# Performance work log

Measured on AMD Instinct MI355X. Metric: run time of the kernel, lower is better.

Reference implementation:

```python
import jax, jax.numpy as jnp
import numpy as np

VOL_SHAPE = (256, 256, 256)
DELTA = 1
EPS = 1e-8


def _radius_bins(shape, delta):
    # Frequency-index radius map (equivalent to distance from DC with fft wraparound),
    # binned into shells of width `delta`. Computed once with numpy (constant).
    axes = [np.fft.fftfreq(n) * n for n in shape]
    grids = np.meshgrid(*axes, indexing='ij')
    r = np.sqrt(sum(g.astype(np.float64) ** 2 for g in grids))
    bins = np.floor(r / delta).astype(np.int32)
    return bins.ravel(), int(bins.max()) + 1

_BINS, _NUM_SHELLS = _radius_bins(VOL_SHAPE, DELTA)
_BINS_J = jnp.asarray(_BINS)


def setup_inputs() -> dict:
    key = jax.random.key(0)
    kx, ky = jax.random.split(key)
    shp = (2, 1) + VOL_SHAPE
    X = jax.random.normal(kx, shp, dtype=jnp.float32)
    Y = jax.random.normal(ky, shp, dtype=jnp.float32)
    return {"X": X, "Y": Y}


def _fsc(X, Y):
    B, C = X.shape[0], X.shape[1]
    Fx = jnp.fft.fftn(X, axes=(-3, -2, -1))  # complex64 [B,C,D,H,W]
    Fy = jnp.fft.fftn(Y, axes=(-3, -2, -1))
    N = VOL_SHAPE[0] * VOL_SHAPE[1] * VOL_SHAPE[2]
    # Per-voxel quantities, flattened over the volume: [B*C, N]
    num = (Fx.real * Fy.real + Fx.imag * Fy.imag).reshape(B * C, N)  # Re(Fx * conj(Fy))
    px = (Fx.real ** 2 + Fx.imag ** 2).reshape(B * C, N)
    py = (Fy.real ** 2 + Fy.imag ** 2).reshape(B * C, N)
    seg = lambda v: jax.ops.segment_sum(v, _BINS_J, num_segments=_NUM_SHELLS)
    num_s = jax.vmap(seg)(num)  # [B*C, S]
    px_s = jax.vmap(seg)(px)
    py_s = jax.vmap(seg)(py)
    fsc = num_s / jnp.sqrt(px_s * py_s + EPS)  # [B*C, S]
    return fsc.reshape(B, C, _NUM_SHELLS)


def reference(X, Y):
    fsc = _fsc(X, Y)
    # size_average=True: average over radii, channel and batch -> scalar
    return jnp.mean(fsc)
```

## Files before the change

### kernel.cpp

```cpp
#include <hip/hip_runtime.h>
#include <math.h>

#define VOL (256 * 256 * 256)
#define NSHELL 222
#define SBINS 224
#define NSPLIT 16
#define PI_D 3.14159265358979323846
#define VSTRIDE ((size_t)129 << 16)

__device__ __forceinline__ int rev4(int e) {
  return ((e & 3) << 6) | (((e >> 2) & 3) << 4) | (((e >> 4) & 3) << 2) | ((e >> 6) & 3);
}

__global__ void tw_init(float2* __restrict__ gtw) {
  int t = threadIdx.x;
  double a = -2.0 * PI_D * (double)t / 256.0;
  gtw[t] = make_float2((float)cos(a), (float)sin(a));
}

__device__ __forceinline__ void bfly4_dif(float* re, float* im, const float* twr,
                                          const float* twi, int a0, int a1, int a2,
                                          int a3, int t1, int t2, int t3) {
  float x0r = re[a0], x0i = im[a0], x1r = re[a1], x1i = im[a1];
  float x2r = re[a2], x2i = im[a2], x3r = re[a3], x3i = im[a3];
  float s02r = x0r + x2r, s02i = x0i + x2i, d02r = x0r - x2r, d02i = x0i - x2i;
  float s13r = x1r + x3r, s13i = x1i + x3i, d13r = x1r - x3r, d13i = x1i - x3i;
  re[a0] = s02r + s13r; im[a0] = s02i + s13i;
  float c1r = d02r + d13i, c1i = d02i - d13r;
  re[a1] = c1r * twr[t1] - c1i * twi[t1]; im[a1] = c1r * twi[t1] + c1i * twr[t1];
  float c2r = s02r - s13r, c2i = s02i - s13i;
  re[a2] = c2r * twr[t2] - c2i * twi[t2]; im[a2] = c2r * twi[t2] + c2i * twr[t2];
  float c3r = d02r - d13i, c3i = d02i + d13r;
  re[a3] = c3r * twr[t3] - c3i * twi[t3]; im[a3] = c3r * twi[t3] + c3i * twr[t3];
}

__device__ __forceinline__ void seg_flush(float* sh, int sb, float nv, float pv,
                                          float qv, int l) {
#pragma unroll
  for (int d = 1; d < 64; d <<= 1) {
    int sbo = __shfl_down(sb, d);
    float no = __shfl_down(nv, d);
    float po = __shfl_down(pv, d);
    float qo = __shfl_down(qv, d);
    if (l + d < 64 && sbo == sb) { nv += no; pv += po; qv += qo; }
  }
  int sbp = __shfl_up(sb, 1);
  if (l == 0 || sbp != sb) {
    atomicAdd(&sh[3 * sb + 0], nv);
    atomicAdd(&sh[3 * sb + 1], pv);
    atomicAdd(&sh[3 * sb + 2], qv);
  }
}

__device__ __forceinline__ float2 cmul(float2 a, float2 b) {
  return make_float2(a.x * b.x - a.y * b.y, a.x * b.y + a.y * b.x);
}

__device__ __forceinline__ void fft16(float2* v) {
  const float C1 = 0.92387953251128674f;
  const float S1 = 0.38268343236508978f;
  const float R2 = 0.70710678118654752f;
  float2 s[16];
#pragma unroll
  for (int p = 0; p < 4; ++p) {
    float2 a = v[p], b = v[p + 4], cc = v[p + 8], d = v[p + 12];
    float2 t0 = make_float2(a.x + cc.x, a.y + cc.y);
    float2 t2 = make_float2(a.x - cc.x, a.y - cc.y);
    float2 t1 = make_float2(b.x + d.x, b.y + d.y);
    float2 t3 = make_float2(b.x - d.x, b.y - d.y);
    s[p]      = make_float2(t0.x + t1.x, t0.y + t1.y);
    s[p + 4]  = make_float2(t2.x + t3.y, t2.y - t3.x);
    s[p + 8]  = make_float2(t0.x - t1.x, t0.y - t1.y);
    s[p + 12] = make_float2(t2.x - t3.y, t2.y + t3.x);
  }
  s[5]  = cmul(s[5],  make_float2(C1, -S1));
  s[6]  = cmul(s[6],  make_float2(R2, -R2));
  s[7]  = cmul(s[7],  make_float2(S1, -C1));
  s[9]  = cmul(s[9],  make_float2(R2, -R2));
  s[10] = cmul(s[10], make_float2(0.f, -1.f));
  s[11] = cmul(s[11], make_float2(-R2, -R2));
  s[13] = cmul(s[13], make_float2(S1, -C1));
  s[14] = cmul(s[14], make_float2(-R2, -R2));
  s[15] = cmul(s[15], make_float2(-C1, S1));
#pragma unroll
  for (int r = 0; r < 4; ++r) {
    float2 u0 = s[4 * r], u1 = s[4 * r + 1], u2 = s[4 * r + 2], u3 = s[4 * r + 3];
    float2 e0 = make_float2(u0.x + u2.x, u0.y + u2.y);
    float2 e1 = make_float2(u0.x - u2.x, u0.y - u2.y);
    float2 o0 = make_float2(u1.x + u3.x, u1.y + u3.y);
    float2 o1 = make_float2(u1.x - u3.x, u1.y - u3.y);
    v[r]      = make_float2(e0.x + o0.x, e0.y + o0.y);
    v[4 + r]  = make_float2(e1.x + o1.y, e1.y - o1.x);
    v[8 + r]  = make_float2(e0.x - o0.x, e0.y - o0.y);
    v[12 + r] = make_float2(e1.x - o1.y, e1.y + o1.x);
  }
}

__global__ __launch_bounds__(256) void fft_z_pack(const float* __restrict__ X,
                                                  const float* __restrict__ Y,
                                                  float2* __restrict__ Gx,
                                                  float2* __restrict__ Gy,
                                                  const float2* __restrict__ gtw) {
  __shared__ float zr[256 * 17], zi[256 * 17];
  __shared__ float twr[256], twi[256];
  int t = threadIdx.x;
  { float2 w = gtw[t]; twr[t] = w.x; twi[t] = w.y; }
  int li = t >> 4, c = t & 15;
  int y = blockIdx.x >> 4;
  int x0 = (blockIdx.x & 15) << 4;
  const float4* xp = (const float4*)(X + (((size_t)(x0 + li)) << 16) + ((size_t)y << 8));
  const float4* yp = (const float4*)(Y + (((size_t)(x0 + li)) << 16) + ((size_t)y << 8));
#pragma unroll
  for (int it = 0; it < 4; ++it) {
    int e4 = c + 16 * it;
    float4 a = xp[e4];
    float4 b = yp[e4];
    int e = e4 << 2;
    zr[(e + 0) * 17 + li] = a.x; zi[(e + 0) * 17 + li] = b.x;
    zr[(e + 1) * 17 + li] = a.y; zi[(e + 1) * 17 + li] = b.y;
    zr[(e + 2) * 17 + li] = a.z; zi[(e + 2) * 17 + li] = b.z;
    zr[(e + 3) * 17 + li] = a.w; zi[(e + 3) * 17 + li] = b.w;
  }
  __syncthreads();
#pragma unroll
  for (int s = 0; s < 4; ++s) {
    int M = 64 >> (2 * s);
    int F = 1 << (2 * s);
#pragma unroll
    for (int ib = 0; ib < 4; ++ib) {
      int j = c + 16 * ib;
      int p = j & (M - 1);
      int jb = j >> (6 - 2 * s);
      int base = jb * (M << 2) + p;
      bfly4_dif(zr, zi, twr, twi, base * 17 + li, (base + M) * 17 + li,
                (base + 2 * M) * 17 + li, (base + 3 * M) * 17 + li,
                (p * F) & 255, (2 * p * F) & 255, (3 * p * F) & 255);
    }
    __syncthreads();
  }
  int krow = t >> 4, xi = t & 15;
#pragma unroll
  for (int g = 0; g < 9; ++g) {
    int kz = g * 16 + krow;
    if (kz <= 128) {
      int s1 = rev4(kz & 255);
      int s2 = rev4((256 - kz) & 255);
      float ar = zr[s1 * 17 + xi], ai = zi[s1 * 17 + xi];
      float br = zr[s2 * 17 + xi], bi = zi[s2 * 17 + xi];
      size_t off = ((size_t)kz << 16) + ((size_t)y << 8) + (size_t)(x0 + xi);
      Gx[off] = make_float2(0.5f * (ar + br), 0.5f * (ai - bi));
      Gy[off] = make_float2(0.5f * (ai + bi), 0.5f * (br - ar));
    }
  }
}

__global__ __launch_bounds__(256, 4) void fft_y(float2* __restrict__ G,
                                                const float2* __restrict__ gtw) {
  __shared__ float2 scr[16 * 273];
  int t = threadIdx.x;
  int xi = t & 15, h = t >> 4;
  int x0 = blockIdx.x << 4;
  int kz = blockIdx.y;
  float2* Gp = G + (size_t)blockIdx.z * VSTRIDE + ((size_t)kz << 16) + (size_t)(x0 + xi);
  float2 v[16];
#pragma unroll
  for (int m = 0; m < 16; ++m) v[m] = Gp[(size_t)((m << 4) | h) << 8];
  fft16(v);
#pragma unroll
  for (int k1 = 1; k1 < 16; ++k1) v[k1] = cmul(v[k1], gtw[h * k1]);
  int wb = xi * 273 + h * 17;
#pragma unroll
  for (int k1 = 0; k1 < 16; ++k1) scr[wb + k1] = v[k1];
  __syncthreads();
  float2 u[16];
  int rb = xi * 273 + h;
#pragma unroll
  for (int j2 = 0; j2 < 16; ++j2) u[j2] = scr[rb + j2 * 17];
  fft16(u);
#pragma unroll
  for (int k2 = 0; k2 < 16; ++k2) Gp[(size_t)((k2 << 4) | h) << 8] = u[k2];
}

__global__ __launch_bounds__(256, 4) void fft_x_reduce(const float2* __restrict__ G,
                                                       double* __restrict__ sums,
                                                       const float2* __restrict__ gtw) {
  __shared__ float2 pool[4672];
  __shared__ float sh[3 * SBINS];
  int t = threadIdx.x;
  for (int i = t; i < 3 * SBINS; i += 256) sh[i] = 0.f;
  int vol = t >> 7, tt = t & 127;
  int g = tt >> 4, c = tt & 15;
  int kz = blockIdx.y;
  int r0 = blockIdx.x << 3;
  const float2* Gp = G + (size_t)vol * VSTRIDE + ((size_t)kz << 16) + ((size_t)(r0 + g) << 8);
  float2 v[16];
#pragma unroll
  for (int m = 0; m < 16; ++m) v[m] = Gp[(m << 4) | c];
  fft16(v);
#pragma unroll
  for (int k1 = 1; k1 < 16; ++k1) v[k1] = cmul(v[k1], gtw[c * k1]);
  {
    int sbase = ((vol << 3) | g) * 280;
#pragma unroll
    for (int k1 = 0; k1 < 16; ++k1) pool[sbase + c * 17 + k1] = v[k1];
    float2 u[16];
#pragma unroll
    for (int j2 = 0; j2 < 16; ++j2) u[j2] = pool[sbase + j2 * 17 + c];
    fft16(u);
    __syncthreads();
    float2* A = pool + vol * 2336;
#pragma unroll
    for (int k2 = 0; k2 < 16; ++k2) {
      int kx = (k2 << 4) | c;
      A[kx * 9 + k2 + g] = u[k2];
    }
  }
  __syncthreads();
  int fz = kz - ((kz & 128) ? 256 : 0);
  int fz2 = fz * fz;
  int w = t >> 6, l = t & 63;
  const float2* Ax = pool;
  const float2* Ay = pool + 2336;
#pragma unroll
  for (int rr = 0; rr < 2; ++rr) {
    int row = (w << 1) | rr;
    int ky = r0 + row;
    int fy = ky - ((ky & 128) ? 256 : 0);
    int c2 = fy * fy + fz2;
#pragma unroll
    for (int pass = 0; pass < 2; ++pass) {
      int kx = (pass << 6) | l;
      float2 xv = Ax[kx * 9 + (kx >> 4) + row];
      float2 yv = Ay[kx * 9 + (kx >> 4) + row];
      float nv = xv.x * yv.x + xv.y * yv.y;
      float pv = xv.x * xv.x + xv.y * xv.y;
      float qv = yv.x * yv.x + yv.y * yv.y;
      if (kx != 0) {
        int mk = 256 - kx;
        float2 mx = Ax[mk * 9 + (mk >> 4) + row];
        float2 my = Ay[mk * 9 + (mk >> 4) + row];
        nv += mx.x * my.x + mx.y * my.y;
        pv += mx.x * mx.x + mx.y * mx.y;
        qv += my.x * my.x + my.y * my.y;
      }
      int m = kx * kx + c2;
      int sb = (int)sqrtf((float)m);
      while (sb * sb > m) --sb;
      while ((sb + 1) * (sb + 1) <= m) ++sb;
      seg_flush(sh, sb, nv, pv, qv, l);
    }
    if (l == 0) {
      float2 xv = Ax[128 * 9 + 8 + row];
      float2 yv = Ay[128 * 9 + 8 + row];
      int m = 16384 + c2;
      int sb = (int)sqrtf((float)m);
      while (sb * sb > m) --sb;
      while ((sb + 1) * (sb + 1) <= m) ++sb;
      atomicAdd(&sh[3 * sb + 0], xv.x * yv.x + xv.y * yv.y);
      atomicAdd(&sh[3 * sb + 1], xv.x * xv.x + xv.y * xv.y);
      atomicAdd(&sh[3 * sb + 2], yv.x * yv.x + yv.y * yv.y);
    }
  }
  __syncthreads();
  float wf = (kz == 0 || kz == 128) ? 1.f : 2.f;
  double* sp = sums + (size_t)(blockIdx.x & (NSPLIT - 1)) * (3 * SBINS);
  for (int i = t; i < 3 * SBINS; i += 256) {
    float vv = sh[i];
    if (vv != 0.f) atomicAdd(&sp[i], (double)(wf * vv));
  }
}

__global__ void finalize(const double* __restrict__ sums, float* __restrict__ out) {
  __shared__ double red[2 * 3 * SBINS];
  int t = threadIdx.x;
  for (int i = t; i < 2 * 3 * SBINS; i += 256) {
    int b = i / (3 * SBINS), k = i - b * (3 * SBINS);
    const double* s = sums + (size_t)b * NSPLIT * 3 * SBINS + k;
    double a = 0.0;
#pragma unroll
    for (int sp = 0; sp < NSPLIT; ++sp) a += s[(size_t)sp * 3 * SBINS];
    red[i] = a;
  }
  __syncthreads();
  if (t == 0) {
    double acc = 0.0;
    for (int b = 0; b < 2; ++b) {
      const double* s = red + b * 3 * SBINS;
      for (int k = 0; k < NSHELL; ++k)
        acc += s[3 * k] / sqrt(s[3 * k + 1] * s[3 * k + 2] + 1e-8);
    }
    out[0] = (float)(acc / (2.0 * (double)NSHELL));
  }
}

extern "C" void kernel_launch(void* const* d_in, const int* in_sizes, int n_in,
                              void* d_out, int out_size, void* d_ws, size_t ws_size,
                              hipStream_t stream) {
  const float* X = (const float*)d_in[0];
  const float* Y = (const float*)d_in[1];
  float2* Gx = (float2*)d_ws;
  float2* Gy = Gx + VSTRIDE;
  double* sums = (double*)((char*)d_ws + (size_t)2 * VSTRIDE * sizeof(float2));
  float2* gtw = (float2*)(sums + (size_t)2 * NSPLIT * 3 * SBINS);

  hipMemsetAsync(sums, 0, (size_t)2 * NSPLIT * 3 * SBINS * sizeof(double), stream);
  tw_init<<<1, 256, 0, stream>>>(gtw);

  for (int b = 0; b < 2; ++b) {
    fft_z_pack<<<4096, 256, 0, stream>>>(X + (size_t)b * VOL, Y + (size_t)b * VOL, Gx, Gy, gtw);
    fft_y<<<dim3(16, 129, 2), 256, 0, stream>>>(Gx, gtw);
    fft_x_reduce<<<dim3(32, 129), 256, 0, stream>>>(Gx, sums + (size_t)b * NSPLIT * 3 * SBINS, gtw);
  }
  finalize<<<1, 256, 0, stream>>>(sums, (float*)d_out);
}
```

Before: 611.1 us.

## Replace shared-memory radix-4 z-FFT with register four-step 16x16 FFT

The z-axis FFT in fft_z_pack changes from four shared-memory radix-4 DIF stages, each ending in a block barrier, to a register-resident four-step 16x16 decomposition. Each thread does a 16-point FFT in registers, applies twiddles and transposes through a skewed float2 LDS buffer, then does a second 16-point FFT. This removes most barriers and separate re/im LDS traffic, and the output comes out in natural order so the digit-reversal indexing goes away. The kernel also gets a minimum-occupancy launch bound. Between the two passes it relies on ordering within a wavefront instead of barriers, which is only safe because each 16-thread group sits inside a single wave.

```diff
diff --git a/kernel.cpp b/kernel.cpp
--- a/kernel.cpp
+++ b/kernel.cpp
@@ -8,30 +8,10 @@
 #define PI_D 3.14159265358979323846
 #define VSTRIDE ((size_t)129 << 16)
 
-__device__ __forceinline__ int rev4(int e) {
-  return ((e & 3) << 6) | (((e >> 2) & 3) << 4) | (((e >> 4) & 3) << 2) | ((e >> 6) & 3);
-}
-
 __global__ void tw_init(float2* __restrict__ gtw) {
   int t = threadIdx.x;
   double a = -2.0 * PI_D * (double)t / 256.0;
   gtw[t] = make_float2((float)cos(a), (float)sin(a));
-}
-
-__device__ __forceinline__ void bfly4_dif(float* re, float* im, const float* twr,
-                                          const float* twi, int a0, int a1, int a2,
-                                          int a3, int t1, int t2, int t3) {
-  float x0r = re[a0], x0i = im[a0], x1r = re[a1], x1i = im[a1];
-  float x2r = re[a2], x2i = im[a2], x3r = re[a3], x3i = im[a3];
-  float s02r = x0r + x2r, s02i = x0i + x2i, d02r = x0r - x2r, d02i = x0i - x2i;
-  float s13r = x1r + x3r, s13i = x1i + x3i, d13r = x1r - x3r, d13i = x1i - x3i;
-  re[a0] = s02r + s13r; im[a0] = s02i + s13i;
-  float c1r = d02r + d13i, c1i = d02i - d13r;
-  re[a1] = c1r * twr[t1] - c1i * twi[t1]; im[a1] = c1r * twi[t1] + c1i * twr[t1];
-  float c2r = s02r - s13r, c2i = s02i - s13i;
-  re[a2] = c2r * twr[t2] - c2i * twi[t2]; im[a2] = c2r * twi[t2] + c2i * twr[t2];
-  float c3r = d02r - d13i, c3i = d02i + d13r;
-  re[a3] = c3r * twr[t3] - c3i * twi[t3]; im[a3] = c3r * twi[t3] + c3i * twr[t3];
 }
 
 __device__ __forceinline__ void seg_flush(float* sh, int sb, float nv, float pv,
@@ -96,15 +76,13 @@
   }
 }
 
-__global__ __launch_bounds__(256) void fft_z_pack(const float* __restrict__ X,
-                                                  const float* __restrict__ Y,
-                                                  float2* __restrict__ Gx,
-                                                  float2* __restrict__ Gy,
-                                                  const float2* __restrict__ gtw) {
-  __shared__ float zr[256 * 17], zi[256 * 17];
-  __shared__ float twr[256], twi[256];
-  int t = threadIdx.x;
-  { float2 w = gtw[t]; twr[t] = w.x; twi[t] = w.y; }
+__global__ __launch_bounds__(256, 4) void fft_z_pack(const float* __restrict__ X,
+                                                     const float* __restrict__ Y,
+                                                     float2* __restrict__ Gx,
+                                                     float2* __restrict__ Gy,
+                                                     const float2* __restrict__ gtw) {
+  __shared__ float2 zs[256 * 17];
+  int t = threadIdx.x;
   int li = t >> 4, c = t & 15;
   int y = blockIdx.x >> 4;
   int x0 = (blockIdx.x & 15) << 4;
@@ -112,44 +90,41 @@
   const float4* yp = (const float4*)(Y + (((size_t)(x0 + li)) << 16) + ((size_t)y << 8));
 #pragma unroll
   for (int it = 0; it < 4; ++it) {
-    int e4 = c + 16 * it;
-    float4 a = xp[e4];
-    float4 b = yp[e4];
-    int e = e4 << 2;
-    zr[(e + 0) * 17 + li] = a.x; zi[(e + 0) * 17 + li] = b.x;
-    zr[(e + 1) * 17 + li] = a.y; zi[(e + 1) * 17 + li] = b.y;
-    zr[(e + 2) * 17 + li] = a.z; zi[(e + 2) * 17 + li] = b.z;
-    zr[(e + 3) * 17 + li] = a.w; zi[(e + 3) * 17 + li] = b.w;
-  }
-  __syncthreads();
-#pragma unroll
-  for (int s = 0; s < 4; ++s) {
-    int M = 64 >> (2 * s);
-    int F = 1 << (2 * s);
-#pragma unroll
-    for (int ib = 0; ib < 4; ++ib) {
-      int j = c + 16 * ib;
-      int p = j & (M - 1);
-      int jb = j >> (6 - 2 * s);
-      int base = jb * (M << 2) + p;
-      bfly4_dif(zr, zi, twr, twi, base * 17 + li, (base + M) * 17 + li,
-                (base + 2 * M) * 17 + li, (base + 3 * M) * 17 + li,
-                (p * F) & 255, (2 * p * F) & 255, (3 * p * F) & 255);
-    }
-    __syncthreads();
-  }
-  int krow = t >> 4, xi = t & 15;
+    float4 a = xp[c + 16 * it];
+    float4 b = yp[c + 16 * it];
+    int z0 = 4 * c + 64 * it;
+    zs[(z0 + 0) * 17 + li] = make_float2(a.x, b.x);
+    zs[(z0 + 1) * 17 + li] = make_float2(a.y, b.y);
+    zs[(z0 + 2) * 17 + li] = make_float2(a.z, b.z);
+    zs[(z0 + 3) * 17 + li] = make_float2(a.w, b.w);
+  }
+  float2 v[16];
+#pragma unroll
+  for (int m = 0; m < 16; ++m) v[m] = zs[(16 * m + c) * 17 + li];
+  fft16(v);
+#pragma unroll
+  for (int k1 = 1; k1 < 16; ++k1) v[k1] = cmul(v[k1], gtw[c * k1]);
+#pragma unroll
+  for (int k1 = 0; k1 < 16; ++k1) zs[(16 * c + ((k1 + c) & 15)) * 17 + li] = v[k1];
+  float2 u[16];
+#pragma unroll
+  for (int j2 = 0; j2 < 16; ++j2) u[j2] = zs[(16 * j2 + ((c + j2) & 15)) * 17 + li];
+  fft16(u);
+#pragma unroll
+  for (int k2 = 0; k2 < 16; ++k2) zs[(16 * k2 + c) * 17 + li] = u[k2];
+  __syncthreads();
+  int xo = t & 15, ko = t >> 4;
+  float2* gx = Gx + ((size_t)y << 8) + (size_t)(x0 + xo);
+  float2* gy = Gy + ((size_t)y << 8) + (size_t)(x0 + xo);
 #pragma unroll
   for (int g = 0; g < 9; ++g) {
-    int kz = g * 16 + krow;
+    int kz = 16 * g + ko;
     if (kz <= 128) {
-      int s1 = rev4(kz & 255);
-      int s2 = rev4((256 - kz) & 255);
-      float ar = zr[s1 * 17 + xi], ai = zi[s1 * 17 + xi];
-      float br = zr[s2 * 17 + xi], bi = zi[s2 * 17 + xi];
-      size_t off = ((size_t)kz << 16) + ((size_t)y << 8) + (size_t)(x0 + xi);
-      Gx[off] = make_float2(0.5f * (ar + br), 0.5f * (ai - bi));
-      Gy[off] = make_float2(0.5f * (ai + bi), 0.5f * (br - ar));
+      float2 a = zs[kz * 17 + xo];
+      float2 b = zs[((256 - kz) & 255) * 17 + xo];
+      size_t off = (size_t)kz << 16;
+      gx[off] = make_float2(0.5f * (a.x + b.x), 0.5f * (a.y - b.y));
+      gy[off] = make_float2(0.5f * (a.y + b.y), 0.5f * (b.x - a.x));
     }
   }
 }
```

New measurement: 603.6 us. Within noise of the previous version (-1.2%).
